# Performance work log

Hardware: AMD Instinct MI355X
Metric: run time of the kernel (lower is better)

## Reference

```python
import jax, jax.numpy as jnp
import numpy as np


def setup_inputs() -> dict:
    key = jax.random.key(0)
    k1, k2 = jax.random.split(key)
    B, I, O = 16384, 1024, 4096
    return {
        "input": jax.random.normal(k1, (B, I), dtype=jnp.float32),
        "centers": jax.random.normal(k2, (O, I), dtype=jnp.float32),
        "log_sigma": jnp.zeros((O,), dtype=jnp.float32),
    }


def reference(input, centers, log_sigma):
    # as the torch broadcast-subtract-square-sum, without the (B,O,I) intermediate)
    x_sq = jnp.sum(input * input, axis=-1, keepdims=True)        # [B, 1]
    c_sq = jnp.sum(centers * centers, axis=-1)                   # [O]
    cross = input @ centers.T                                     # [B, O]
    d2 = jnp.maximum(x_sq + c_sq[None, :] - 2.0 * cross, 0.0)     # [B, O]
    sigma = jnp.exp(log_sigma)                                    # [O]
    return jnp.exp(-d2 / (2.0 * sigma * sigma)[None, :])
```

## Files before the change

### kernel.cpp

```cpp
#include <hip/hip_runtime.h>
#include <hip/hip_bf16.h>
#include <stdint.h>

#define TM 16384
#define TN 4096
#define TK 1024

#define NT (TK / 64)
#define JT 4

typedef __attribute__((ext_vector_type(8))) short bf16x8;
typedef __attribute__((ext_vector_type(4))) float f32x4;

static __device__ __forceinline__ ushort f2bf(float x) {
    __hip_bfloat16 h = __float2bfloat16(x);
    return *reinterpret_cast<ushort*>(&h);
}

__global__ __launch_bounds__(256) void rowsq_cvt(const float* __restrict__ src,
                                                 ushort* __restrict__ dst,
                                                 float* __restrict__ sq) {
    const int row = blockIdx.x;
    const int t = threadIdx.x;
    const size_t base = (size_t)row * TK + (size_t)t * 4;
    const f32x4 v = __builtin_nontemporal_load((const f32x4*)(src + base));
    float s = v.x * v.x + v.y * v.y + v.z * v.z + v.w * v.w;

    ushort4 b;
    b.x = f2bf(v.x); b.y = f2bf(v.y); b.z = f2bf(v.z); b.w = f2bf(v.w);
    *(ushort4*)(dst + base) = b;

#pragma unroll
    for (int off = 32; off > 0; off >>= 1) s += __shfl_down(s, off);

    __shared__ float red[4];
    const int lane = t & 63, wave = t >> 6;
    if (lane == 0) red[wave] = s;
    __syncthreads();
    if (t == 0) sq[row] = red[0] + red[1] + red[2] + red[3];
}

__global__ __launch_bounds__(256) void scale_k(const float* __restrict__ ls,
                                               float* __restrict__ f) {
    const int i = blockIdx.x * 256 + threadIdx.x;
    if (i < TN) f[i] = -0.5f * expf(-2.0f * ls[i]);
}


#define STAGE(PAN, SRC, H) do {                                                \
    __builtin_amdgcn_global_load_lds(                                          \
        (const __attribute__((address_space(1))) void*)((SRC) + (size_t)(H) * 128 * TK), \
        (__attribute__((address_space(3))) void*)((PAN) + (H) * 8192 + wbase), \
        16, 0, 0);                                                             \
    __builtin_amdgcn_global_load_lds(                                          \
        (const __attribute__((address_space(1))) void*)((SRC) + (size_t)(H) * 128 * TK + 64 * TK), \
        (__attribute__((address_space(3))) void*)((PAN) + (H) * 8192 + 4096 + wbase), \
        16, 0, 0);                                                             \
} while (0)

#define ASRC(S) (gAl + (size_t)(((S) & 63) >> 4) * (256 * (size_t)TK) + (size_t)((S) & 15) * 64)
#define BSRC(S) (gBl + (size_t)((S) & 15) * 64)

#define READA(PAN, QM) do {                                                    \
    _Pragma("unroll") for (int _i = 0; _i < 4; ++_i)                           \
    _Pragma("unroll") for (int _k = 0; _k < 2; ++_k)                           \
        af[_i][_k] = *(const bf16x8*)((PAN) +                                  \
            (size_t)(rowA + (QM) * 64 + _i * 16) * 64 + (cX ^ (_k * 32)));     \
} while (0)

#define READB(PAN, QN) do {                                                    \
    _Pragma("unroll") for (int _n = 0; _n < 2; ++_n)                           \
    _Pragma("unroll") for (int _k = 0; _k < 2; ++_k)                           \
        bf[(QN) * 2 + _n][_k] = *(const bf16x8*)((PAN) +                       \
            (size_t)(rowB + (QN) * 32 + _n * 16) * 64 + (cX ^ (_k * 32)));     \
} while (0)

#define MFMA16(QM, QN)                                                         \
    _Pragma("unroll") for (int _i = 0; _i < 4; ++_i)                           \
    _Pragma("unroll") for (int _n = 0; _n < 2; ++_n)                           \
    _Pragma("unroll") for (int _k = 0; _k < 2; ++_k)                           \
        acc[(QM) * 4 + _i][(QN) * 2 + _n] =                                    \
            __builtin_amdgcn_mfma_f32_16x16x32_bf16(                           \
                af[_i][_k], bf[(QN) * 2 + _n][_k],                             \
                acc[(QM) * 4 + _i][(QN) * 2 + _n], 0, 0, 0)

#define PH_SYNC do {                                                           \
    __builtin_amdgcn_s_barrier();                                              \
    asm volatile("s_waitcnt lgkmcnt(0)" ::: "memory");                         \
    __builtin_amdgcn_sched_barrier(0);                                         \
    __builtin_amdgcn_s_setprio(1);                                             \
} while (0)

#define PH_END do {                                                            \
    __builtin_amdgcn_s_setprio(0);                                             \
    __builtin_amdgcn_s_barrier();                                              \
} while (0)

#define PH_END_VM do {                                                         \
    __builtin_amdgcn_s_setprio(0);                                             \
    asm volatile("s_waitcnt vmcnt(4)" ::: "memory");                           \
    __builtin_amdgcn_s_barrier();                                              \
} while (0)

__global__ __launch_bounds__(512) void rbf_gemm(const ushort* __restrict__ Cb,
                                                const ushort* __restrict__ Xb,
                                                const float* __restrict__ xsq,
                                                const float* __restrict__ csq,
                                                const float* __restrict__ fsc,
                                                float* __restrict__ out) {
    __shared__ __align__(16) ushort lds[65536];

    const int bid = blockIdx.x;
    const int wg = (bid & 7) * 32 + (bid >> 3);
    const int bm = wg >> 2;
    const int jbase = (wg & 3) * 4;
    const int rowx0 = bm * 256;

    const int tid = threadIdx.x;
    const int lane = tid & 63, wave = tid >> 6;
    const int wr = wave >> 2, wc = wave & 3;
    const int lrow = lane & 15, lhi = lane >> 4;
    const int cX = (lhi * 8) ^ ((lrow & 4) << 2) ^ ((lrow & 8) << 2);
    const int rowA = wr * 128 + lrow;
    const int rowB = wc * 64 + lrow;
    const int wbase = wave * 512;

    const int srow = tid >> 3;
    const int scol = ((tid & 7) * 8) ^ ((tid & 32) >> 1) ^ ((tid & 64) >> 1);
    const ushort* gAl = Cb + (size_t)(jbase * 256 + srow) * TK + scol;
    const ushort* gBl = Xb + (size_t)(rowx0 + srow) * TK + scol;

    ushort* pA0 = lds;
    ushort* pB0 = lds + 16384;
    ushort* pA1 = lds + 32768;
    ushort* pB1 = lds + 49152;

    bf16x8 af[4][2];
    bf16x8 bf[4][2];

    STAGE(pB0, BSRC(0), 0); STAGE(pB0, BSRC(0), 1);
    STAGE(pA0, ASRC(0), 0); STAGE(pA0, ASRC(0), 1);
    STAGE(pB1, BSRC(1), 0); STAGE(pB1, BSRC(1), 1);
    asm volatile("s_waitcnt vmcnt(4)" ::: "memory");
    __builtin_amdgcn_s_barrier();

#pragma unroll 1
    for (int j = 0; j < JT; ++j) {
        f32x4 acc[8][4];
#pragma unroll
        for (int m = 0; m < 8; ++m)
#pragma unroll
            for (int n = 0; n < 4; ++n)
                acc[m][n] = (f32x4){0.f, 0.f, 0.f, 0.f};

#pragma unroll 1
        for (int t = 0; t < NT; t += 2) {
            const int s = j * NT + t;

            READA(pA0, 0); READB(pB0, 0);
            STAGE(pA1, ASRC(s + 1), 0);
            PH_SYNC; MFMA16(0, 0); PH_END;

            READB(pB0, 1);
            STAGE(pA1, ASRC(s + 1), 1);
            PH_SYNC; MFMA16(0, 1); PH_END;

            READA(pA0, 1);
            STAGE(pB0, BSRC(s + 2), 0);
            PH_SYNC; MFMA16(1, 0); PH_END;

            STAGE(pB0, BSRC(s + 2), 1);
            PH_SYNC; MFMA16(1, 1); PH_END_VM;

            READA(pA1, 0); READB(pB1, 0);
            STAGE(pA0, ASRC(s + 2), 0);
            PH_SYNC; MFMA16(0, 0); PH_END;

            READB(pB1, 1);
            STAGE(pA0, ASRC(s + 2), 1);
            PH_SYNC; MFMA16(0, 1); PH_END;

            READA(pA1, 1);
            STAGE(pB1, BSRC(s + 3), 0);
            PH_SYNC; MFMA16(1, 0); PH_END;

            STAGE(pB1, BSRC(s + 3), 1);
            PH_SYNC; MFMA16(1, 1); PH_END_VM;
        }

        const int o0 = (jbase + j) * 256 + wr * 128;
        const int b0 = rowx0 + wc * 64;
#pragma unroll
        for (int m = 0; m < 8; ++m) {
            const int o4 = o0 + m * 16 + lhi * 4;
            const f32x4 cs4 = *(const f32x4*)(csq + o4);
            const f32x4 fs4 = *(const f32x4*)(fsc + o4);
#pragma unroll
            for (int n = 0; n < 4; ++n) {
                const int b = b0 + n * 16 + lrow;
                const float xs = xsq[b];
                f32x4 v;
#pragma unroll
                for (int jj = 0; jj < 4; ++jj) {
                    float d2 = fmaxf(xs + cs4[jj] - 2.0f * acc[m][n][jj], 0.0f);
                    v[jj] = __expf(fs4[jj] * d2);
                }
                *(f32x4*)(out + (size_t)b * TN + o4) = v;
            }
        }
    }
}

extern "C" void kernel_launch(void* const* d_in, const int* in_sizes, int n_in,
                              void* d_out, int out_size, void* d_ws, size_t ws_size,
                              hipStream_t stream) {
    const float* inp = (const float*)d_in[0];
    const float* ctr = (const float*)d_in[1];
    const float* ls  = (const float*)d_in[2];
    float* out = (float*)d_out;

    ushort* Abf = (ushort*)d_ws;
    ushort* Bbf = Abf + (size_t)TM * TK;
    float* xsq = (float*)(Bbf + (size_t)TN * TK);
    float* csq = xsq + TM;
    float* fsc = csq + TN;

    rowsq_cvt<<<TM, 256, 0, stream>>>(inp, Abf, xsq);
    rowsq_cvt<<<TN, 256, 0, stream>>>(ctr, Bbf, csq);
    scale_k<<<(TN + 255) / 256, 256, 0, stream>>>(ls, fsc);

    rbf_gemm<<<256, 512, 0, stream>>>(Bbf, Abf, xsq, csq, fsc, out);
}
```

Measured before the change: 190.4 us.

## Use 4 waves with 128x128 per-wave tiles and prefetched LDS fragments

Cuts the GEMM workgroup from 8 waves to 4, so each wave now owns a 128x128 output tile (8x8 MFMA accumulators) instead of 128x64. This raises register-level reuse of A/B fragments per LDS read. Fragment reads are double-buffered (af0/af1), and the next stage's first fragments are loaded before the barrier, so the per-phase lgkmcnt wait is dropped. Each thread now issues more global_load_lds ops per stage. Register pressure rises sharply (256 accumulator floats plus fragments), which risks spills, and fewer waves leaves less latency hiding.

```diff
diff --git a/kernel.cpp b/kernel.cpp
--- a/kernel.cpp
+++ b/kernel.cpp
@@ -47,67 +47,73 @@
 }
 
 
-#define STAGE(PAN, SRC, H) do {                                                \
+#define STAGEQ(PAN, SRC, Q)                                                    \
     __builtin_amdgcn_global_load_lds(                                          \
-        (const __attribute__((address_space(1))) void*)((SRC) + (size_t)(H) * 128 * TK), \
-        (__attribute__((address_space(3))) void*)((PAN) + (H) * 8192 + wbase), \
-        16, 0, 0);                                                             \
-    __builtin_amdgcn_global_load_lds(                                          \
-        (const __attribute__((address_space(1))) void*)((SRC) + (size_t)(H) * 128 * TK + 64 * TK), \
-        (__attribute__((address_space(3))) void*)((PAN) + (H) * 8192 + 4096 + wbase), \
-        16, 0, 0);                                                             \
+        (const __attribute__((address_space(1))) void*)((SRC) + (size_t)(Q) * 32 * TK), \
+        (__attribute__((address_space(3))) void*)((PAN) + (Q) * 2048 + wbase), \
+        16, 0, 0)
+
+#define STAGE4(PAN, SRC, H) do {                                               \
+    STAGEQ(PAN, SRC, (H) * 4 + 0); STAGEQ(PAN, SRC, (H) * 4 + 1);              \
+    STAGEQ(PAN, SRC, (H) * 4 + 2); STAGEQ(PAN, SRC, (H) * 4 + 3);              \
 } while (0)
 
 #define ASRC(S) (gAl + (size_t)(((S) & 63) >> 4) * (256 * (size_t)TK) + (size_t)((S) & 15) * 64)
 #define BSRC(S) (gBl + (size_t)((S) & 15) * 64)
 
-#define READA(PAN, QM) do {                                                    \
+#define READAQ(DST, PAN, QM) do {                                              \
     _Pragma("unroll") for (int _i = 0; _i < 4; ++_i)                           \
     _Pragma("unroll") for (int _k = 0; _k < 2; ++_k)                           \
-        af[_i][_k] = *(const bf16x8*)((PAN) +                                  \
+        DST[_i][_k] = *(const bf16x8*)((PAN) +                                 \
             (size_t)(rowA + (QM) * 64 + _i * 16) * 64 + (cX ^ (_k * 32)));     \
 } while (0)
 
-#define READB(PAN, QN) do {                                                    \
-    _Pragma("unroll") for (int _n = 0; _n < 2; ++_n)                           \
+#define READBH(PAN, NH) do {                                                   \
+    _Pragma("unroll") for (int _n = 0; _n < 4; ++_n)                           \
     _Pragma("unroll") for (int _k = 0; _k < 2; ++_k)                           \
-        bf[(QN) * 2 + _n][_k] = *(const bf16x8*)((PAN) +                       \
-            (size_t)(rowB + (QN) * 32 + _n * 16) * 64 + (cX ^ (_k * 32)));     \
-} while (0)
-
-#define MFMA16(QM, QN)                                                         \
+        bf[(NH) * 4 + _n][_k] = *(const bf16x8*)((PAN) +                       \
+            (size_t)(rowB + (NH) * 64 + _n * 16) * 64 + (cX ^ (_k * 32)));     \
+} while (0)
+
+#define MFMA32(AF, QM, QN)                                                     \
     _Pragma("unroll") for (int _i = 0; _i < 4; ++_i)                           \
-    _Pragma("unroll") for (int _n = 0; _n < 2; ++_n)                           \
+    _Pragma("unroll") for (int _n = 0; _n < 4; ++_n)                           \
     _Pragma("unroll") for (int _k = 0; _k < 2; ++_k)                           \
-        acc[(QM) * 4 + _i][(QN) * 2 + _n] =                                    \
+        acc[(QM) * 4 + _i][(QN) * 4 + _n] =                                    \
             __builtin_amdgcn_mfma_f32_16x16x32_bf16(                           \
-                af[_i][_k], bf[(QN) * 2 + _n][_k],                             \
-                acc[(QM) * 4 + _i][(QN) * 2 + _n], 0, 0, 0)
+                AF[_i][_k], bf[(QN) * 4 + _n][_k],                             \
+                acc[(QM) * 4 + _i][(QN) * 4 + _n], 0, 0, 0)
 
 #define PH_SYNC do {                                                           \
     __builtin_amdgcn_s_barrier();                                              \
-    asm volatile("s_waitcnt lgkmcnt(0)" ::: "memory");                         \
     __builtin_amdgcn_sched_barrier(0);                                         \
     __builtin_amdgcn_s_setprio(1);                                             \
 } while (0)
 
 #define PH_END do {                                                            \
     __builtin_amdgcn_s_setprio(0);                                             \
+    __builtin_amdgcn_sched_barrier(0);                                         \
     __builtin_amdgcn_s_barrier();                                              \
 } while (0)
 
-#define PH_END_VM do {                                                         \
+#define PH_VM do {                                                             \
     __builtin_amdgcn_s_setprio(0);                                             \
-    asm volatile("s_waitcnt vmcnt(4)" ::: "memory");                           \
+    asm volatile("s_waitcnt vmcnt(8)" ::: "memory");                           \
+    __builtin_amdgcn_sched_barrier(0);                                         \
+} while (0)
+
+#define PH_BAR do {                                                            \
+    __builtin_amdgcn_sched_barrier(0);                                         \
     __builtin_amdgcn_s_barrier();                                              \
 } while (0)
 
-__global__ __launch_bounds__(512) void rbf_gemm(const ushort* __restrict__ Cb,
-                                                const ushort* __restrict__ Xb,
-                                                const float* __restrict__ xsq,
-                                                const float* __restrict__ csq,
-                                                const float* __restrict__ fsc,
-                                                float* __restrict__ out) {
+__global__ __launch_bounds__(256, 1) void rbf_gemm(
+        const ushort* __restrict__ Cb,
+        const ushort* __restrict__ Xb,
+        const float* __restrict__ xsq,
+        const float* __restrict__ csq,
+        const float* __restrict__ fsc,
+        float* __restrict__ out) {
     __shared__ __align__(16) ushort lds[65536];
 
     const int bid = blockIdx.x;
@@ -118,11 +124,11 @@
 
     const int tid = threadIdx.x;
     const int lane = tid & 63, wave = tid >> 6;
-    const int wr = wave >> 2, wc = wave & 3;
+    const int wr = wave >> 1, wc = wave & 1;
     const int lrow = lane & 15, lhi = lane >> 4;
     const int cX = (lhi * 8) ^ ((lrow & 4) << 2) ^ ((lrow & 8) << 2);
     const int rowA = wr * 128 + lrow;
-    const int rowB = wc * 64 + lrow;
+    const int rowB = wc * 128 + lrow;
     const int wbase = wave * 512;
 
     const int srow = tid >> 3;
@@ -135,68 +141,65 @@
     ushort* pA1 = lds + 32768;
     ushort* pB1 = lds + 49152;
 
-    bf16x8 af[4][2];
-    bf16x8 bf[4][2];
-
-    STAGE(pB0, BSRC(0), 0); STAGE(pB0, BSRC(0), 1);
-    STAGE(pA0, ASRC(0), 0); STAGE(pA0, ASRC(0), 1);
-    STAGE(pB1, BSRC(1), 0); STAGE(pB1, BSRC(1), 1);
-    asm volatile("s_waitcnt vmcnt(4)" ::: "memory");
+    bf16x8 af0[4][2], af1[4][2];
+    bf16x8 bf[8][2];
+
+    STAGE4(pB0, BSRC(0), 0); STAGE4(pB0, BSRC(0), 1);
+    STAGE4(pA0, ASRC(0), 0); STAGE4(pA0, ASRC(0), 1);
+    STAGE4(pB1, BSRC(1), 0); STAGE4(pB1, BSRC(1), 1);
+    asm volatile("s_waitcnt vmcnt(8)" ::: "memory");
     __builtin_amdgcn_s_barrier();
+    READAQ(af0, pA0, 0); READBH(pB0, 0);
 
 #pragma unroll 1
     for (int j = 0; j < JT; ++j) {
-        f32x4 acc[8][4];
+        f32x4 acc[8][8];
 #pragma unroll
         for (int m = 0; m < 8; ++m)
 #pragma unroll
-            for (int n = 0; n < 4; ++n)
+            for (int n = 0; n < 8; ++n)
                 acc[m][n] = (f32x4){0.f, 0.f, 0.f, 0.f};
 
 #pragma unroll 1
         for (int t = 0; t < NT; t += 2) {
             const int s = j * NT + t;
 
-            READA(pA0, 0); READB(pB0, 0);
-            STAGE(pA1, ASRC(s + 1), 0);
-            PH_SYNC; MFMA16(0, 0); PH_END;
-
-            READB(pB0, 1);
-            STAGE(pA1, ASRC(s + 1), 1);
-            PH_SYNC; MFMA16(0, 1); PH_END;
-
-            READA(pA0, 1);
-            STAGE(pB0, BSRC(s + 2), 0);
-            PH_SYNC; MFMA16(1, 0); PH_END;
-
-            STAGE(pB0, BSRC(s + 2), 1);
-            PH_SYNC; MFMA16(1, 1); PH_END_VM;
-
-            READA(pA1, 0); READB(pB1, 0);
-            STAGE(pA0, ASRC(s + 2), 0);
-            PH_SYNC; MFMA16(0, 0); PH_END;
-
-            READB(pB1, 1);
-            STAGE(pA0, ASRC(s + 2), 1);
-            PH_SYNC; MFMA16(0, 1); PH_END;
-
-            READA(pA1, 1);
-            STAGE(pB1, BSRC(s + 3), 0);
-            PH_SYNC; MFMA16(1, 0); PH_END;
-
-            STAGE(pB1, BSRC(s + 3), 1);
-            PH_SYNC; MFMA16(1, 1); PH_END_VM;
+            READAQ(af1, pA0, 1); READBH(pB0, 1);
+            STAGE4(pA1, ASRC(s + 1), 0);
+            PH_SYNC; MFMA32(af0, 0, 0); PH_END;
+            STAGE4(pA1, ASRC(s + 1), 1);
+            PH_SYNC; MFMA32(af0, 0, 1); PH_END;
+            STAGE4(pB0, BSRC(s + 2), 0);
+            PH_SYNC; MFMA32(af1, 1, 0); PH_END;
+            STAGE4(pB0, BSRC(s + 2), 1);
+            PH_SYNC; MFMA32(af1, 1, 1);
+            PH_VM;
+            READAQ(af0, pA1, 0); READBH(pB1, 0);
+            PH_BAR;
+
+            READAQ(af1, pA1, 1); READBH(pB1, 1);
+            STAGE4(pA0, ASRC(s + 2), 0);
+            PH_SYNC; MFMA32(af0, 0, 0); PH_END;
+            STAGE4(pA0, ASRC(s + 2), 1);
+            PH_SYNC; MFMA32(af0, 0, 1); PH_END;
+            STAGE4(pB1, BSRC(s + 3), 0);
+            PH_SYNC; MFMA32(af1, 1, 0); PH_END;
+            STAGE4(pB1, BSRC(s + 3), 1);
+            PH_SYNC; MFMA32(af1, 1, 1);
+            PH_VM;
+            READAQ(af0, pA0, 0); READBH(pB0, 0);
+            PH_BAR;
         }
 
         const int o0 = (jbase + j) * 256 + wr * 128;
-        const int b0 = rowx0 + wc * 64;
+        const int b0 = rowx0 + wc * 128;
 #pragma unroll
         for (int m = 0; m < 8; ++m) {
             const int o4 = o0 + m * 16 + lhi * 4;
             const f32x4 cs4 = *(const f32x4*)(csq + o4);
             const f32x4 fs4 = *(const f32x4*)(fsc + o4);
 #pragma unroll
-            for (int n = 0; n < 4; ++n) {
+            for (int n = 0; n < 8; ++n) {
                 const int b = b0 + n * 16 + lrow;
                 const float xs = xsq[b];
                 f32x4 v;
@@ -229,5 +232,5 @@
     rowsq_cvt<<<TN, 256, 0, stream>>>(ctr, Bbf, csq);
     scale_k<<<(TN + 255) / 256, 256, 0, stream>>>(ls, fsc);
 
-    rbf_gemm<<<256, 512, 0, stream>>>(Bbf, Abf, xsq, csq, fsc, out);
-}
+    rbf_gemm<<<256, 256, 0, stream>>>(Bbf, Abf, xsq, csq, fsc, out);
+}
```

Measured after the change: 484.0 us. 2.54x slower.

## Launch one workgroup per 256x256 output tile instead of four-tile persistent loop

Applied to the files above, without the earlier changes.

Each workgroup previously walked four consecutive 256-wide output-column tiles in an outer loop, keeping the double-buffered LDS pipeline running across tile boundaries. Now the grid has one workgroup per output tile, 1024 in total, with a single K loop and epilogue each, and the block-to-XCD swizzle is adjusted to match. The aim is finer-grained scheduling and simpler per-block control flow. In exchange, every block repeats the prologue loads. Loads for the next tile no longer overlap the current epilogue. With 128 KB of LDS per block, only one block fits on a CU, so blocks run in several waves.

```diff
diff --git a/kernel.cpp b/kernel.cpp
--- a/kernel.cpp
+++ b/kernel.cpp
@@ -7,7 +7,6 @@
 #define TK 1024
 
 #define NT (TK / 64)
-#define JT 4
 
 typedef __attribute__((ext_vector_type(8))) short bf16x8;
 typedef __attribute__((ext_vector_type(4))) float f32x4;
@@ -58,7 +57,7 @@
         16, 0, 0);                                                             \
 } while (0)
 
-#define ASRC(S) (gAl + (size_t)(((S) & 63) >> 4) * (256 * (size_t)TK) + (size_t)((S) & 15) * 64)
+#define ASRC(S) (gAl + (size_t)((S) & 15) * 64)
 #define BSRC(S) (gBl + (size_t)((S) & 15) * 64)
 
 #define READA(PAN, QM) do {                                                    \
@@ -102,18 +101,19 @@
     __builtin_amdgcn_s_barrier();                                              \
 } while (0)
 
-__global__ __launch_bounds__(512) void rbf_gemm(const ushort* __restrict__ Cb,
-                                                const ushort* __restrict__ Xb,
-                                                const float* __restrict__ xsq,
-                                                const float* __restrict__ csq,
-                                                const float* __restrict__ fsc,
-                                                float* __restrict__ out) {
+__global__ __launch_bounds__(512) void rbf_gemm(
+        const ushort* __restrict__ Cb,
+        const ushort* __restrict__ Xb,
+        const float* __restrict__ xsq,
+        const float* __restrict__ csq,
+        const float* __restrict__ fsc,
+        float* __restrict__ out) {
     __shared__ __align__(16) ushort lds[65536];
 
     const int bid = blockIdx.x;
-    const int wg = (bid & 7) * 32 + (bid >> 3);
-    const int bm = wg >> 2;
-    const int jbase = (wg & 3) * 4;
+    const int wg = (bid & 7) * 128 + (bid >> 3);
+    const int bm = wg >> 4;
+    const int bn = wg & 15;
     const int rowx0 = bm * 256;
 
     const int tid = threadIdx.x;
@@ -127,7 +127,7 @@
 
     const int srow = tid >> 3;
     const int scol = ((tid & 7) * 8) ^ ((tid & 32) >> 1) ^ ((tid & 64) >> 1);
-    const ushort* gAl = Cb + (size_t)(jbase * 256 + srow) * TK + scol;
+    const ushort* gAl = Cb + (size_t)(bn * 256 + srow) * TK + scol;
     const ushort* gBl = Xb + (size_t)(rowx0 + srow) * TK + scol;
 
     ushort* pA0 = lds;
@@ -137,6 +137,13 @@
 
     bf16x8 af[4][2];
     bf16x8 bf[4][2];
+
+    f32x4 acc[8][4];
+#pragma unroll
+    for (int m = 0; m < 8; ++m)
+#pragma unroll
+        for (int n = 0; n < 4; ++n)
+            acc[m][n] = (f32x4){0.f, 0.f, 0.f, 0.f};
 
     STAGE(pB0, BSRC(0), 0); STAGE(pB0, BSRC(0), 1);
     STAGE(pA0, ASRC(0), 0); STAGE(pA0, ASRC(0), 1);
@@ -145,68 +152,56 @@
     __builtin_amdgcn_s_barrier();
 
 #pragma unroll 1
-    for (int j = 0; j < JT; ++j) {
-        f32x4 acc[8][4];
-#pragma unroll
-        for (int m = 0; m < 8; ++m)
-#pragma unroll
-            for (int n = 0; n < 4; ++n)
-                acc[m][n] = (f32x4){0.f, 0.f, 0.f, 0.f};
-
-#pragma unroll 1
-        for (int t = 0; t < NT; t += 2) {
-            const int s = j * NT + t;
-
-            READA(pA0, 0); READB(pB0, 0);
-            STAGE(pA1, ASRC(s + 1), 0);
-            PH_SYNC; MFMA16(0, 0); PH_END;
-
-            READB(pB0, 1);
-            STAGE(pA1, ASRC(s + 1), 1);
-            PH_SYNC; MFMA16(0, 1); PH_END;
-
-            READA(pA0, 1);
-            STAGE(pB0, BSRC(s + 2), 0);
-            PH_SYNC; MFMA16(1, 0); PH_END;
-
-            STAGE(pB0, BSRC(s + 2), 1);
-            PH_SYNC; MFMA16(1, 1); PH_END_VM;
-
-            READA(pA1, 0); READB(pB1, 0);
-            STAGE(pA0, ASRC(s + 2), 0);
-            PH_SYNC; MFMA16(0, 0); PH_END;
-
-            READB(pB1, 1);
-            STAGE(pA0, ASRC(s + 2), 1);
-            PH_SYNC; MFMA16(0, 1); PH_END;
-
-            READA(pA1, 1);
-            STAGE(pB1, BSRC(s + 3), 0);
-            PH_SYNC; MFMA16(1, 0); PH_END;
-
-            STAGE(pB1, BSRC(s + 3), 1);
-            PH_SYNC; MFMA16(1, 1); PH_END_VM;
-        }
-
-        const int o0 = (jbase + j) * 256 + wr * 128;
-        const int b0 = rowx0 + wc * 64;
-#pragma unroll
-        for (int m = 0; m < 8; ++m) {
-            const int o4 = o0 + m * 16 + lhi * 4;
-            const f32x4 cs4 = *(const f32x4*)(csq + o4);
-            const f32x4 fs4 = *(const f32x4*)(fsc + o4);
-#pragma unroll
-            for (int n = 0; n < 4; ++n) {
-                const int b = b0 + n * 16 + lrow;
-                const float xs = xsq[b];
-                f32x4 v;
-#pragma unroll
-                for (int jj = 0; jj < 4; ++jj) {
-                    float d2 = fmaxf(xs + cs4[jj] - 2.0f * acc[m][n][jj], 0.0f);
-                    v[jj] = __expf(fs4[jj] * d2);
-                }
-                *(f32x4*)(out + (size_t)b * TN + o4) = v;
+    for (int t = 0; t < NT; t += 2) {
+        READA(pA0, 0); READB(pB0, 0);
+        STAGE(pA1, ASRC(t + 1), 0);
+        PH_SYNC; MFMA16(0, 0); PH_END;
+
+        READB(pB0, 1);
+        STAGE(pA1, ASRC(t + 1), 1);
+        PH_SYNC; MFMA16(0, 1); PH_END;
+
+        READA(pA0, 1);
+        STAGE(pB0, BSRC(t + 2), 0);
+        PH_SYNC; MFMA16(1, 0); PH_END;
+
+        STAGE(pB0, BSRC(t + 2), 1);
+        PH_SYNC; MFMA16(1, 1); PH_END_VM;
+
+        READA(pA1, 0); READB(pB1, 0);
+        STAGE(pA0, ASRC(t + 2), 0);
+        PH_SYNC; MFMA16(0, 0); PH_END;
+
+        READB(pB1, 1);
+        STAGE(pA0, ASRC(t + 2), 1);
+        PH_SYNC; MFMA16(0, 1); PH_END;
+
+        READA(pA1, 1);
+        STAGE(pB1, BSRC(t + 3), 0);
+        PH_SYNC; MFMA16(1, 0); PH_END;
+
+        STAGE(pB1, BSRC(t + 3), 1);
+        PH_SYNC; MFMA16(1, 1); PH_END_VM;
+    }
+
+    const int o0 = bn * 256 + wr * 128;
+    const int b0 = rowx0 + wc * 64;
+#pragma unroll
+    for (int m = 0; m < 8; ++m) {
+        const int o4 = o0 + m * 16 + lhi * 4;
+        const f32x4 cs4 = *(const f32x4*)(csq + o4);
+        const f32x4 fs4 = *(const f32x4*)(fsc + o4);
+#pragma unroll
+        for (int n = 0; n < 4; ++n) {
+            const int b = b0 + n * 16 + lrow;
+            const float xs = xsq[b];
+            f32x4 v;
+#pragma unroll
+            for (int jj = 0; jj < 4; ++jj) {
+                float d2 = fmaxf(xs + cs4[jj] - 2.0f * acc[m][n][jj], 0.0f);
+                v[jj] = __expf(fs4[jj] * d2);
             }
+            *(f32x4*)(out + (size_t)b * TN + o4) = v;
         }
     }
 }
@@ -229,5 +224,5 @@
     rowsq_cvt<<<TN, 256, 0, stream>>>(ctr, Bbf, csq);
     scale_k<<<(TN + 255) / 256, 256, 0, stream>>>(ls, fsc);
 
-    rbf_gemm<<<256, 512, 0, stream>>>(Bbf, Abf, xsq, csq, fsc, out);
-}
+    rbf_gemm<<<(TM / 256) * (TN / 256), 512, 0, stream>>>(Bbf, Abf, xsq, csq, fsc, out);
+}
```

Result: no change. 187.5 us (-1.5%).
